# Kernel optimization log

Measured on AMD Instinct MI355X. Metric: run time of the kernel, lower is better.

The kernel has to match this reference:

```python
import jax, jax.numpy as jnp
import numpy as np

D = 128
K = 8
TEMPERATURE = 1.0
LN_EPS = 1e-5
NORM_EPS = 1e-12


def setup_inputs() -> dict:
    key = jax.random.key(0)
    ks = jax.random.split(key, 6)
    B = 262144
    global_prosody = jax.random.normal(ks[0], (B, D), dtype=jnp.float32)
    W = jax.random.normal(ks[1], (D, D), dtype=jnp.float32) / np.sqrt(D)
    b = jnp.zeros((D,), dtype=jnp.float32)
    gamma = jnp.ones((D,), dtype=jnp.float32)
    beta = jnp.zeros((D,), dtype=jnp.float32)
    # codebook initialized as rows of an orthonormal basis (SVD of random init)
    init = jax.random.normal(ks[2], (D, K), dtype=jnp.float32)
    U, _, _ = jnp.linalg.svd(init, full_matrices=False)
    codebook = U[:, :K].T  # (K, D)
    return {"global_prosody": global_prosody, "W": W, "b": b,
            "gamma": gamma, "beta": beta, "codebook": codebook}


def _l2norm(x, axis=-1):
    n = jnp.sqrt(jnp.sum(x * x, axis=axis, keepdims=True))
    return x / jnp.maximum(n, NORM_EPS)


def reference(global_prosody, W, b, gamma, beta, codebook):
    # proj: Linear + LayerNorm
    h = global_prosody @ W.T + b                      # (B, D)
    mu = jnp.mean(h, axis=-1, keepdims=True)
    var = jnp.var(h, axis=-1, keepdims=True)
    h = (h - mu) / jnp.sqrt(var + LN_EPS) * gamma + beta
    # cosine-sim logits
    h_norm = _l2norm(h)                               # (B, D)
    cb_norm = _l2norm(codebook)                       # (K, D)
    logits = (h_norm @ cb_norm.T) / TEMPERATURE       # (B, K)
    soft_assign = jax.nn.softmax(logits, axis=-1)
    hard_indices = jnp.argmax(logits, axis=-1)        # (B,)
    hard_assign = jax.nn.one_hot(hard_indices, K, dtype=jnp.float32)
    # straight-through assignment
    assign = hard_assign + soft_assign - jax.lax.stop_gradient(soft_assign)
    embedding = assign @ codebook                     # (B, D)
    return hard_indices, soft_assign, embedding, logits
```

## Files before the change

kernel.cpp:

```cpp
#include <hip/hip_runtime.h>
#include <math.h>

#define DD 128
#define KK 8
#define LN_EPS 1e-5f
#define NORM_EPS 1e-12f

typedef __attribute__((ext_vector_type(8))) short bf16x8;
typedef __attribute__((ext_vector_type(16))) float f32x16;
typedef unsigned int uint;
typedef unsigned short ushort;

#define G2B_OFF_F   (122880 / 4)
#define SCAL_OFF_F  (123904 / 4)

__device__ inline void split3(float x, uint& h, uint& m, uint& l) {
    uint u0 = __float_as_uint(x);
    uint rh = (u0 + 0x7FFFu + ((u0 >> 16) & 1u)) & 0xFFFF0000u;
    float xh = __uint_as_float(rh);
    float r1 = x - xh;
    uint u1 = __float_as_uint(r1);
    uint rm = (u1 + 0x7FFFu + ((u1 >> 16) & 1u)) & 0xFFFF0000u;
    float xm = __uint_as_float(rm);
    float r2 = r1 - xm;
    uint u2 = __float_as_uint(r2);
    uint rl = (u2 + 0x7FFFu + ((u2 >> 16) & 1u));
    h = rh; m = rm; l = rl;
}

__device__ inline void split3t(float x, uint& h, uint& m, uint& l) {
    uint u0 = __float_as_uint(x);
    float xh = __uint_as_float(u0 & 0xFFFF0000u);
    float r1 = x - xh;
    uint u1 = __float_as_uint(r1);
    float xm = __uint_as_float(u1 & 0xFFFF0000u);
    float r2 = r1 - xm;
    h = u0; m = u1; l = __float_as_uint(r2);
}

__device__ inline uint packhi(uint a1, uint a0) {
    return __builtin_amdgcn_perm(a1, a0, 0x07060302u);
}

__device__ inline void split2packt(float e0, float e1, uint& ph, uint& pm, uint& pl) {
    uint h0, m0, l0, h1, m1, l1;
    split3t(e0, h0, m0, l0);
    split3t(e1, h1, m1, l1);
    ph = packhi(h1, h0);
    pm = packhi(m1, m0);
    pl = packhi(l1, l0);
}

union FragU  { uint4 u; bf16x8 f; };
union AccU16 { f32x16 v; float a[16]; };

__global__ void l1q_prep0(const float* __restrict__ b, const float* __restrict__ gamma,
                          const float* __restrict__ beta, const float* __restrict__ cb,
                          float* __restrict__ ws)
{
    __shared__ float invn_s[KK];
    const int t = threadIdx.x;
    if (t < KK) {
        float s = 0.f;
        for (int j = 0; j < DD; ++j) { float v = cb[t * DD + j]; s = fmaf(v, v, s); }
        invn_s[t] = 1.0f / fmaxf(sqrtf(s), NORM_EPS);
    }
    __syncthreads();
    {
        float g = gamma[t];
        float* g2b = ws + G2B_OFF_F;
        g2b[2 * t]     = g * g;
        g2b[2 * t + 1] = b[t];
    }
    float* scal = ws + SCAL_OFF_F;
    if (t < KK) {
        float in = invn_s[t];
        float p = 0.f, q = 0.f, cu = 0.f;
        for (int j = 0; j < DD; ++j) {
            float c = cb[t * DD + j] * in;
            p  = fmaf(c, gamma[j], p);
            q  = fmaf(c, beta[j], q);
            cu = fmaf(c * gamma[j], b[j], cu);
        }
        scal[t]      = p;
        scal[8 + t]  = q;
        scal[22 + t] = cu;
    }
    if (t == 16) { float s = 0.f; for (int j = 0; j < DD; ++j) { float g = gamma[j]; s = fmaf(g, g, s); } scal[16] = s; }
    if (t == 17) { float s = 0.f; for (int j = 0; j < DD; ++j) s = fmaf(gamma[j], beta[j], s); scal[17] = s; }
    if (t == 18) { float s = 0.f; for (int j = 0; j < DD; ++j) { float v = beta[j]; s = fmaf(v, v, s); } scal[18] = s; }
    if (t == 19) { float s = 0.f; for (int j = 0; j < DD; ++j) s += b[j]; scal[19] = s; }
    if (t == 20) { float s = 0.f; for (int j = 0; j < DD; ++j) s = fmaf(gamma[j] * gamma[j], b[j], s); scal[20] = s; }
    if (t == 21) { float s = 0.f; for (int j = 0; j < DD; ++j) s = fmaf(gamma[j] * beta[j], b[j], s); scal[21] = s; }
}

__global__ void l1q_prepA(const float* __restrict__ W, const float* __restrict__ b,
                          const float* __restrict__ gamma, const float* __restrict__ beta,
                          const float* __restrict__ cb, ushort* __restrict__ wsA)
{
    __shared__ float invn_s[KK];
    __shared__ float we[11][DD];
    __shared__ float wext[32][16];
    const int t = threadIdx.x;
    const int jt = blockIdx.x >> 3;
    const int ks = blockIdx.x & 7;

    if (jt == 4) {
        if (t < KK) {
            float s = 0.f;
            for (int j = 0; j < DD; ++j) { float v = cb[t * DD + j]; s = fmaf(v, v, s); }
            invn_s[t] = 1.0f / fmaxf(sqrtf(s), NORM_EPS);
        }
        __syncthreads();
        for (int idx = t; idx < 11 * DD; idx += 256) {
            int e = idx / DD, j = idx % DD;
            float g = gamma[j];
            float v;
            if (e == 0)      v = 1.0f;
            else if (e == 1) v = g * g;
            else if (e == 2) v = g * beta[j];
            else             v = cb[(e - 3) * DD + j] * invn_s[e - 3] * g;
            we[e][j] = v;
        }
        __syncthreads();
    }

    for (int idx = t; idx < 512; idx += 256) {
        int jl = idx >> 4, kk = idx & 15;
        int k = ks * 16 + kk;
        float val;
        if (jt < 4) {
            val = W[(jt * 32 + jl) * DD + k];
        } else if (jl < 11) {
            float s = 0.f;
            for (int j = 0; j < DD; ++j) s = fmaf(we[jl][j], W[j * DD + k], s);
            val = s;
        } else {
            val = 0.f;
        }
        wext[jl][kk] = val;
    }
    __syncthreads();

    for (int idx = t; idx < 512; idx += 256) {
        int jl = idx >> 4, kk = idx & 15;
        int lane = jl + 32 * (kk >> 3);
        int i = kk & 7;
        uint h, m, l;
        split3(wext[jl][kk], h, m, l);
        int base = jt * 8 + ks;
        wsA[(0 * 40 + base) * 512 + lane * 8 + i] = (ushort)(h >> 16);
        wsA[(1 * 40 + base) * 512 + lane * 8 + i] = (ushort)(m >> 16);
        wsA[(2 * 40 + base) * 512 + lane * 8 + i] = (ushort)(l >> 16);
    }
}

__global__ __launch_bounds__(1024, 4)
void l1q_main(const float* __restrict__ x, const ushort* __restrict__ wsA,
              const float* __restrict__ wsf, const float* __restrict__ cb,
              float* __restrict__ out_idx, float* __restrict__ out_soft,
              float* __restrict__ out_emb, float* __restrict__ out_log,
              int B)
{
    __shared__ uint4 Wl4[7680];
    __shared__ float gath[16][352];
    __shared__ int   besti[16][32];
    __shared__ float g2b_s[256];
    __shared__ float scal_s[32];

    const int t = threadIdx.x;
    const int wave = t >> 6;
    const int lane = t & 63;
    const int n = lane & 31;
    const int h = lane >> 5;
    const int rowbase = blockIdx.x * 512 + wave * 32;
    const int row = rowbase + n;

    const float* xp = x + (size_t)row * DD + h * 8;
    float4 ra = *(const float4*)(xp + 0);
    float4 rc = *(const float4*)(xp + 4);

    {
        const uint4* src = (const uint4*)wsA;
        #pragma unroll
        for (int i = 0; i < 8; ++i) {
            int idx = t + i * 1024;
            if (idx < 7680) Wl4[idx] = src[idx];
        }
    }
    if (t < 256) g2b_s[t] = wsf[G2B_OFF_F + t];
    if (t < 32)  scal_s[t] = wsf[SCAL_OFF_F + t];
    __syncthreads();

    f32x16 acc[5];
    #pragma unroll
    for (int jt = 0; jt < 5; ++jt)
        #pragma unroll
        for (int r = 0; r < 16; ++r) acc[jt][r] = 0.f;

    #pragma unroll
    for (int ks = 0; ks < 8; ++ks) {
        int kn = ks < 7 ? ks + 1 : 7;
        float4 na = *(const float4*)(xp + kn * 16 + 0);
        float4 nc = *(const float4*)(xp + kn * 16 + 4);

        FragU xh, xm, xl;
        split2packt(ra.x, ra.y, xh.u.x, xm.u.x, xl.u.x);
        split2packt(ra.z, ra.w, xh.u.y, xm.u.y, xl.u.y);
        split2packt(rc.x, rc.y, xh.u.z, xm.u.z, xl.u.z);
        split2packt(rc.z, rc.w, xh.u.w, xm.u.w, xl.u.w);

        #pragma unroll
        for (int jt = 0; jt < 5; ++jt) {
            const int pl = jt * 8 + ks;
            FragU wh, wm, wl;
            wh.u = Wl4[(0 * 40 + pl) * 64 + lane];
            wm.u = Wl4[(1 * 40 + pl) * 64 + lane];
            wl.u = Wl4[(2 * 40 + pl) * 64 + lane];
            f32x16 c = acc[jt];
            c = __builtin_amdgcn_mfma_f32_32x32x16_bf16(wl.f, xh.f, c, 0, 0, 0);
            c = __builtin_amdgcn_mfma_f32_32x32x16_bf16(wh.f, xl.f, c, 0, 0, 0);
            c = __builtin_amdgcn_mfma_f32_32x32x16_bf16(wm.f, xm.f, c, 0, 0, 0);
            c = __builtin_amdgcn_mfma_f32_32x32x16_bf16(wm.f, xh.f, c, 0, 0, 0);
            c = __builtin_amdgcn_mfma_f32_32x32x16_bf16(wh.f, xm.f, c, 0, 0, 0);
            c = __builtin_amdgcn_mfma_f32_32x32x16_bf16(wh.f, xh.f, c, 0, 0, 0);
            acc[jt] = c;
        }
        ra = na; rc = nc;
    }

    float s2a = 0.f, t2a = 0.f;
    #pragma unroll
    for (int jt = 0; jt < 4; ++jt) {
        AccU16 a; a.v = acc[jt];
        #pragma unroll
        for (int rq = 0; rq < 4; ++rq) {
            int jb = jt * 32 + 8 * rq + 4 * h;
            #pragma unroll
            for (int r = 0; r < 4; ++r) {
                float2 gb = *(const float2*)&g2b_s[2 * (jb + r)];
                float hv = a.a[rq * 4 + r] + gb.y;
                float h2 = hv * hv;
                s2a += h2;
                t2a = fmaf(gb.x, h2, t2a);
            }
        }
    }
    s2a += __shfl_xor(s2a, 32);
    t2a += __shfl_xor(t2a, 32);

    {
        AccU16 a; a.v = acc[4];
        #pragma unroll
        for (int rq = 0; rq < 4; ++rq) {
            #pragma unroll
            for (int r = 0; r < 4; ++r) {
                int local = r + 8 * rq + 4 * h;
                if (local < 11) gath[wave][n * 11 + local] = a.a[rq * 4 + r];
            }
        }
    }
    __builtin_amdgcn_s_waitcnt(0);
    const float* gp = &gath[wave][n * 11];

    const float inv128 = 1.0f / 128.0f;
    const float cg2s = scal_s[16], cgbs = scal_s[17], cb2s = scal_s[18];

    float s1  = gp[0] + scal_s[19];
    float t1  = gp[1] + scal_s[20];
    float r1v = gp[2] + scal_s[21];
    float u[KK];
    #pragma unroll
    for (int k = 0; k < KK; ++k) u[k] = gp[3 + k] + scal_s[22 + k];

    float mu = s1 * inv128;
    float var = fmaf(-mu, mu, s2a * inv128);
    float istd = 1.0f / sqrtf(var + LN_EPS);
    float nrm2 = istd * istd * (t2a - 2.f * mu * t1 + mu * mu * cg2s)
               + 2.f * istd * (r1v - mu * cgbs) + cb2s;
    float rinv = 1.0f / fmaxf(sqrtf(fmaxf(nrm2, 0.f)), NORM_EPS);

    float lg[KK];
    #pragma unroll
    for (int k = 0; k < KK; ++k)
        lg[k] = (istd * (u[k] - mu * scal_s[k]) + scal_s[8 + k]) * rinv;

    float mx = lg[0]; int bi = 0;
    #pragma unroll
    for (int k = 1; k < KK; ++k) if (lg[k] > mx) { mx = lg[k]; bi = k; }

    float ex[KK], se = 0.f;
    #pragma unroll
    for (int k = 0; k < KK; ++k) { ex[k] = expf(lg[k] - mx); se += ex[k]; }
    float rse = 1.0f / se;

    const int m = rowbase + n;
    if (h == 0) {
        out_idx[m] = (float)bi;
        besti[wave][n] = bi;
        *(float4*)&out_log[(size_t)m * KK]     = make_float4(lg[0], lg[1], lg[2], lg[3]);
        *(float4*)&out_log[(size_t)m * KK + 4] = make_float4(lg[4], lg[5], lg[6], lg[7]);
    } else {
        *(float4*)&out_soft[(size_t)m * KK]     = make_float4(ex[0] * rse, ex[1] * rse, ex[2] * rse, ex[3] * rse);
        *(float4*)&out_soft[(size_t)m * KK + 4] = make_float4(ex[4] * rse, ex[5] * rse, ex[6] * rse, ex[7] * rse);
    }

    __builtin_amdgcn_s_waitcnt(0);
    const float4* cb4 = (const float4*)cb;
    float4* eo = (float4*)out_emb;
    #pragma unroll
    for (int i = 0; i < 16; ++i) {
        int f4 = lane + 64 * i;
        int rl = f4 >> 5;
        int c  = f4 & 31;
        int k0 = besti[wave][rl];
        eo[(size_t)(rowbase + rl) * 32 + c] = cb4[k0 * 32 + c];
    }
}

extern "C" void kernel_launch(void* const* d_in, const int* in_sizes, int n_in,
                              void* d_out, int out_size, void* d_ws, size_t ws_size,
                              hipStream_t stream) {
    const float* x     = (const float*)d_in[0];
    const float* W     = (const float*)d_in[1];
    const float* b     = (const float*)d_in[2];
    const float* gamma = (const float*)d_in[3];
    const float* beta  = (const float*)d_in[4];
    const float* cb    = (const float*)d_in[5];
    const int B = in_sizes[0] / DD;

    float*  ws  = (float*)d_ws;
    ushort* wsA = (ushort*)d_ws;

    float* out    = (float*)d_out;
    float* o_idx  = out;
    float* o_soft = out + (size_t)B;
    float* o_emb  = out + (size_t)B * (1 + KK);
    float* o_log  = out + (size_t)B * (1 + KK + DD);

    hipLaunchKernelGGL(l1q_prep0, dim3(1), dim3(128), 0, stream, b, gamma, beta, cb, ws);
    hipLaunchKernelGGL(l1q_prepA, dim3(40), dim3(256), 0, stream, W, b, gamma, beta, cb, wsA);
    const int grid = B / 512;
    hipLaunchKernelGGL(l1q_main, dim3(grid), dim3(1024), 0, stream,
                       x, wsA, ws, cb, o_idx, o_soft, o_emb, o_log, B);
}
```

Baseline: 297.7 us.

## Process two row tiles per wave, sharing W fragments, and fold prep kernels

Each wave now handles 64 rows as two 32-row tiles, so every W fragment read from LDS feeds two interleaved MFMA chains. All x loads are issued up front, and the grid is halved, which spreads the LDS W staging over twice as many rows. The epilogue swaps the LDS gather and the besti scratch for cross-lane shuffles, and the scalar-prep kernel is merged into prepA to save a launch. The cost is much higher register pressure from 32 float4 x registers plus two accumulator sets, which risks spills or lower occupancy. Fewer blocks also means less latency hiding across blocks.

```diff
diff --git a/kernel.cpp b/kernel.cpp
--- a/kernel.cpp
+++ b/kernel.cpp
@@ -52,51 +52,11 @@
 }
 
 union FragU  { uint4 u; bf16x8 f; };
-union AccU16 { f32x16 v; float a[16]; };
-
-__global__ void l1q_prep0(const float* __restrict__ b, const float* __restrict__ gamma,
-                          const float* __restrict__ beta, const float* __restrict__ cb,
-                          float* __restrict__ ws)
-{
-    __shared__ float invn_s[KK];
-    const int t = threadIdx.x;
-    if (t < KK) {
-        float s = 0.f;
-        for (int j = 0; j < DD; ++j) { float v = cb[t * DD + j]; s = fmaf(v, v, s); }
-        invn_s[t] = 1.0f / fmaxf(sqrtf(s), NORM_EPS);
-    }
-    __syncthreads();
-    {
-        float g = gamma[t];
-        float* g2b = ws + G2B_OFF_F;
-        g2b[2 * t]     = g * g;
-        g2b[2 * t + 1] = b[t];
-    }
-    float* scal = ws + SCAL_OFF_F;
-    if (t < KK) {
-        float in = invn_s[t];
-        float p = 0.f, q = 0.f, cu = 0.f;
-        for (int j = 0; j < DD; ++j) {
-            float c = cb[t * DD + j] * in;
-            p  = fmaf(c, gamma[j], p);
-            q  = fmaf(c, beta[j], q);
-            cu = fmaf(c * gamma[j], b[j], cu);
-        }
-        scal[t]      = p;
-        scal[8 + t]  = q;
-        scal[22 + t] = cu;
-    }
-    if (t == 16) { float s = 0.f; for (int j = 0; j < DD; ++j) { float g = gamma[j]; s = fmaf(g, g, s); } scal[16] = s; }
-    if (t == 17) { float s = 0.f; for (int j = 0; j < DD; ++j) s = fmaf(gamma[j], beta[j], s); scal[17] = s; }
-    if (t == 18) { float s = 0.f; for (int j = 0; j < DD; ++j) { float v = beta[j]; s = fmaf(v, v, s); } scal[18] = s; }
-    if (t == 19) { float s = 0.f; for (int j = 0; j < DD; ++j) s += b[j]; scal[19] = s; }
-    if (t == 20) { float s = 0.f; for (int j = 0; j < DD; ++j) s = fmaf(gamma[j] * gamma[j], b[j], s); scal[20] = s; }
-    if (t == 21) { float s = 0.f; for (int j = 0; j < DD; ++j) s = fmaf(gamma[j] * beta[j], b[j], s); scal[21] = s; }
-}
 
 __global__ void l1q_prepA(const float* __restrict__ W, const float* __restrict__ b,
                           const float* __restrict__ gamma, const float* __restrict__ beta,
-                          const float* __restrict__ cb, ushort* __restrict__ wsA)
+                          const float* __restrict__ cb, ushort* __restrict__ wsA,
+                          float* __restrict__ ws)
 {
     __shared__ float invn_s[KK];
     __shared__ float we[11][DD];
@@ -153,6 +113,112 @@
         wsA[(1 * 40 + base) * 512 + lane * 8 + i] = (ushort)(m >> 16);
         wsA[(2 * 40 + base) * 512 + lane * 8 + i] = (ushort)(l >> 16);
     }
+
+    if (jt == 4 && ks == 0) {
+        if (t < DD) {
+            float g = gamma[t];
+            float* g2b = ws + G2B_OFF_F;
+            g2b[2 * t]     = g * g;
+            g2b[2 * t + 1] = b[t];
+        }
+        float* scal = ws + SCAL_OFF_F;
+        if (t < KK) {
+            float in = invn_s[t];
+            float p = 0.f, q = 0.f, cu = 0.f;
+            for (int j = 0; j < DD; ++j) {
+                float c = cb[t * DD + j] * in;
+                p  = fmaf(c, gamma[j], p);
+                q  = fmaf(c, beta[j], q);
+                cu = fmaf(c * gamma[j], b[j], cu);
+            }
+            scal[t]      = p;
+            scal[8 + t]  = q;
+            scal[22 + t] = cu;
+        }
+        if (t == 16) { float s = 0.f; for (int j = 0; j < DD; ++j) { float g = gamma[j]; s = fmaf(g, g, s); } scal[16] = s; }
+        if (t == 17) { float s = 0.f; for (int j = 0; j < DD; ++j) s = fmaf(gamma[j], beta[j], s); scal[17] = s; }
+        if (t == 18) { float s = 0.f; for (int j = 0; j < DD; ++j) { float v = beta[j]; s = fmaf(v, v, s); } scal[18] = s; }
+        if (t == 19) { float s = 0.f; for (int j = 0; j < DD; ++j) s += b[j]; scal[19] = s; }
+        if (t == 20) { float s = 0.f; for (int j = 0; j < DD; ++j) s = fmaf(gamma[j] * gamma[j], b[j], s); scal[20] = s; }
+        if (t == 21) { float s = 0.f; for (int j = 0; j < DD; ++j) s = fmaf(gamma[j] * beta[j], b[j], s); scal[21] = s; }
+    }
+}
+
+__device__ inline int tile_epilogue(const f32x16* acc, int h, int m,
+                                    const float* g2b_s, const float* scal_s,
+                                    float* __restrict__ out_idx,
+                                    float* __restrict__ out_soft,
+                                    float* __restrict__ out_log)
+{
+    float s2a = 0.f, t2a = 0.f;
+    #pragma unroll
+    for (int jt = 0; jt < 4; ++jt) {
+        #pragma unroll
+        for (int rq = 0; rq < 4; ++rq) {
+            int jb = jt * 32 + 8 * rq + 4 * h;
+            #pragma unroll
+            for (int r = 0; r < 4; ++r) {
+                float2 gb = *(const float2*)&g2b_s[2 * (jb + r)];
+                float hv = acc[jt][rq * 4 + r] + gb.y;
+                float h2 = hv * hv;
+                s2a += h2;
+                t2a = fmaf(gb.x, h2, t2a);
+            }
+        }
+    }
+    s2a += __shfl_xor(s2a, 32);
+    t2a += __shfl_xor(t2a, 32);
+
+    float a0 = acc[4][0], a1 = acc[4][1], a2 = acc[4][2], a3 = acc[4][3];
+    float a4 = acc[4][4], a5 = acc[4][5], a6 = acc[4][6];
+    float o0 = __shfl_xor(a0, 32), o1 = __shfl_xor(a1, 32);
+    float o2 = __shfl_xor(a2, 32), o3 = __shfl_xor(a3, 32);
+    float o4 = __shfl_xor(a4, 32), o5 = __shfl_xor(a5, 32), o6 = __shfl_xor(a6, 32);
+    bool hi = (h != 0);
+    float L0 = hi ? o0 : a0, L1 = hi ? o1 : a1, L2 = hi ? o2 : a2, L3 = hi ? o3 : a3;
+    float L4 = hi ? a0 : o0, L5 = hi ? a1 : o1, L6 = hi ? a2 : o2, L7 = hi ? a3 : o3;
+    float L8 = hi ? o4 : a4, L9 = hi ? o5 : a5, L10 = hi ? o6 : a6;
+
+    const float inv128 = 1.0f / 128.0f;
+    const float cg2s = scal_s[16], cgbs = scal_s[17], cb2s = scal_s[18];
+
+    float s1  = L0 + scal_s[19];
+    float t1  = L1 + scal_s[20];
+    float r1v = L2 + scal_s[21];
+    float u[KK] = {L3 + scal_s[22], L4 + scal_s[23], L5 + scal_s[24],
+                   L6 + scal_s[25], L7 + scal_s[26], L8 + scal_s[27],
+                   L9 + scal_s[28], L10 + scal_s[29]};
+
+    float mu = s1 * inv128;
+    float var = fmaf(-mu, mu, s2a * inv128);
+    float istd = 1.0f / sqrtf(var + LN_EPS);
+    float nrm2 = istd * istd * (t2a - 2.f * mu * t1 + mu * mu * cg2s)
+               + 2.f * istd * (r1v - mu * cgbs) + cb2s;
+    float rinv = 1.0f / fmaxf(sqrtf(fmaxf(nrm2, 0.f)), NORM_EPS);
+
+    float lg[KK];
+    #pragma unroll
+    for (int k = 0; k < KK; ++k)
+        lg[k] = (istd * (u[k] - mu * scal_s[k]) + scal_s[8 + k]) * rinv;
+
+    float mx = lg[0]; int bi = 0;
+    #pragma unroll
+    for (int k = 1; k < KK; ++k) if (lg[k] > mx) { mx = lg[k]; bi = k; }
+
+    float ex[KK], se = 0.f;
+    #pragma unroll
+    for (int k = 0; k < KK; ++k) { ex[k] = expf(lg[k] - mx); se += ex[k]; }
+    float rse = 1.0f / se;
+
+    if (h == 0) {
+        out_idx[m] = (float)bi;
+        *(float4*)&out_log[(size_t)m * KK]     = make_float4(lg[0], lg[1], lg[2], lg[3]);
+        *(float4*)&out_log[(size_t)m * KK + 4] = make_float4(lg[4], lg[5], lg[6], lg[7]);
+    } else {
+        *(float4*)&out_soft[(size_t)m * KK]     = make_float4(ex[0] * rse, ex[1] * rse, ex[2] * rse, ex[3] * rse);
+        *(float4*)&out_soft[(size_t)m * KK + 4] = make_float4(ex[4] * rse, ex[5] * rse, ex[6] * rse, ex[7] * rse);
+    }
+    return bi;
 }
 
 __global__ __launch_bounds__(1024, 4)
@@ -163,22 +229,15 @@
               int B)
 {
     __shared__ uint4 Wl4[7680];
-    __shared__ float gath[16][352];
-    __shared__ int   besti[16][32];
     __shared__ float g2b_s[256];
     __shared__ float scal_s[32];
 
     const int t = threadIdx.x;
+    const int lane = t & 63;
     const int wave = t >> 6;
-    const int lane = t & 63;
     const int n = lane & 31;
     const int h = lane >> 5;
-    const int rowbase = blockIdx.x * 512 + wave * 32;
-    const int row = rowbase + n;
-
-    const float* xp = x + (size_t)row * DD + h * 8;
-    float4 ra = *(const float4*)(xp + 0);
-    float4 rc = *(const float4*)(xp + 4);
+    const int rowbase = blockIdx.x * 1024 + wave * 64;
 
     {
         const uint4* src = (const uint4*)wsA;
@@ -192,23 +251,34 @@
     if (t < 32)  scal_s[t] = wsf[SCAL_OFF_F + t];
     __syncthreads();
 
-    f32x16 acc[5];
+    const float* xpA = x + (size_t)(rowbase + n) * DD + h * 8;
+    const float* xpB = xpA + 32 * DD;
+    float4 xA[16], xB[16];
+    #pragma unroll
+    for (int ks = 0; ks < 8; ++ks) {
+        xA[2 * ks]     = *(const float4*)(xpA + ks * 16);
+        xA[2 * ks + 1] = *(const float4*)(xpA + ks * 16 + 4);
+        xB[2 * ks]     = *(const float4*)(xpB + ks * 16);
+        xB[2 * ks + 1] = *(const float4*)(xpB + ks * 16 + 4);
+    }
+
+    f32x16 accA[5], accB[5];
     #pragma unroll
     for (int jt = 0; jt < 5; ++jt)
         #pragma unroll
-        for (int r = 0; r < 16; ++r) acc[jt][r] = 0.f;
+        for (int r = 0; r < 16; ++r) { accA[jt][r] = 0.f; accB[jt][r] = 0.f; }
 
     #pragma unroll
     for (int ks = 0; ks < 8; ++ks) {
-        int kn = ks < 7 ? ks + 1 : 7;
-        float4 na = *(const float4*)(xp + kn * 16 + 0);
-        float4 nc = *(const float4*)(xp + kn * 16 + 4);
-
-        FragU xh, xm, xl;
-        split2packt(ra.x, ra.y, xh.u.x, xm.u.x, xl.u.x);
-        split2packt(ra.z, ra.w, xh.u.y, xm.u.y, xl.u.y);
-        split2packt(rc.x, rc.y, xh.u.z, xm.u.z, xl.u.z);
-        split2packt(rc.z, rc.w, xh.u.w, xm.u.w, xl.u.w);
+        FragU ah, am, al, bh, bm, bl;
+        split2packt(xA[2 * ks].x,     xA[2 * ks].y,     ah.u.x, am.u.x, al.u.x);
+        split2packt(xA[2 * ks].z,     xA[2 * ks].w,     ah.u.y, am.u.y, al.u.y);
+        split2packt(xA[2 * ks + 1].x, xA[2 * ks + 1].y, ah.u.z, am.u.z, al.u.z);
+        split2packt(xA[2 * ks + 1].z, xA[2 * ks + 1].w, ah.u.w, am.u.w, al.u.w);
+        split2packt(xB[2 * ks].x,     xB[2 * ks].y,     bh.u.x, bm.u.x, bl.u.x);
+        split2packt(xB[2 * ks].z,     xB[2 * ks].w,     bh.u.y, bm.u.y, bl.u.y);
+        split2packt(xB[2 * ks + 1].x, xB[2 * ks + 1].y, bh.u.z, bm.u.z, bl.u.z);
+        split2packt(xB[2 * ks + 1].z, xB[2 * ks + 1].w, bh.u.w, bm.u.w, bl.u.w);
 
         #pragma unroll
         for (int jt = 0; jt < 5; ++jt) {
@@ -217,95 +287,27 @@
             wh.u = Wl4[(0 * 40 + pl) * 64 + lane];
             wm.u = Wl4[(1 * 40 + pl) * 64 + lane];
             wl.u = Wl4[(2 * 40 + pl) * 64 + lane];
-            f32x16 c = acc[jt];
-            c = __builtin_amdgcn_mfma_f32_32x32x16_bf16(wl.f, xh.f, c, 0, 0, 0);
-            c = __builtin_amdgcn_mfma_f32_32x32x16_bf16(wh.f, xl.f, c, 0, 0, 0);
-            c = __builtin_amdgcn_mfma_f32_32x32x16_bf16(wm.f, xm.f, c, 0, 0, 0);
-            c = __builtin_amdgcn_mfma_f32_32x32x16_bf16(wm.f, xh.f, c, 0, 0, 0);
-            c = __builtin_amdgcn_mfma_f32_32x32x16_bf16(wh.f, xm.f, c, 0, 0, 0);
-            c = __builtin_amdgcn_mfma_f32_32x32x16_bf16(wh.f, xh.f, c, 0, 0, 0);
-            acc[jt] = c;
-        }
-        ra = na; rc = nc;
-    }
-
-    float s2a = 0.f, t2a = 0.f;
-    #pragma unroll
-    for (int jt = 0; jt < 4; ++jt) {
-        AccU16 a; a.v = acc[jt];
-        #pragma unroll
-        for (int rq = 0; rq < 4; ++rq) {
-            int jb = jt * 32 + 8 * rq + 4 * h;
-            #pragma unroll
-            for (int r = 0; r < 4; ++r) {
-                float2 gb = *(const float2*)&g2b_s[2 * (jb + r)];
-                float hv = a.a[rq * 4 + r] + gb.y;
-                float h2 = hv * hv;
-                s2a += h2;
-                t2a = fmaf(gb.x, h2, t2a);
-            }
-        }
-    }
-    s2a += __shfl_xor(s2a, 32);
-    t2a += __shfl_xor(t2a, 32);
-
-    {
-        AccU16 a; a.v = acc[4];
-        #pragma unroll
-        for (int rq = 0; rq < 4; ++rq) {
-            #pragma unroll
-            for (int r = 0; r < 4; ++r) {
-                int local = r + 8 * rq + 4 * h;
-                if (local < 11) gath[wave][n * 11 + local] = a.a[rq * 4 + r];
-            }
-        }
-    }
-    __builtin_amdgcn_s_waitcnt(0);
-    const float* gp = &gath[wave][n * 11];
-
-    const float inv128 = 1.0f / 128.0f;
-    const float cg2s = scal_s[16], cgbs = scal_s[17], cb2s = scal_s[18];
-
-    float s1  = gp[0] + scal_s[19];
-    float t1  = gp[1] + scal_s[20];
-    float r1v = gp[2] + scal_s[21];
-    float u[KK];
-    #pragma unroll
-    for (int k = 0; k < KK; ++k) u[k] = gp[3 + k] + scal_s[22 + k];
-
-    float mu = s1 * inv128;
-    float var = fmaf(-mu, mu, s2a * inv128);
-    float istd = 1.0f / sqrtf(var + LN_EPS);
-    float nrm2 = istd * istd * (t2a - 2.f * mu * t1 + mu * mu * cg2s)
-               + 2.f * istd * (r1v - mu * cgbs) + cb2s;
-    float rinv = 1.0f / fmaxf(sqrtf(fmaxf(nrm2, 0.f)), NORM_EPS);
-
-    float lg[KK];
-    #pragma unroll
-    for (int k = 0; k < KK; ++k)
-        lg[k] = (istd * (u[k] - mu * scal_s[k]) + scal_s[8 + k]) * rinv;
-
-    float mx = lg[0]; int bi = 0;
-    #pragma unroll
-    for (int k = 1; k < KK; ++k) if (lg[k] > mx) { mx = lg[k]; bi = k; }
-
-    float ex[KK], se = 0.f;
-    #pragma unroll
-    for (int k = 0; k < KK; ++k) { ex[k] = expf(lg[k] - mx); se += ex[k]; }
-    float rse = 1.0f / se;
-
-    const int m = rowbase + n;
-    if (h == 0) {
-        out_idx[m] = (float)bi;
-        besti[wave][n] = bi;
-        *(float4*)&out_log[(size_t)m * KK]     = make_float4(lg[0], lg[1], lg[2], lg[3]);
-        *(float4*)&out_log[(size_t)m * KK + 4] = make_float4(lg[4], lg[5], lg[6], lg[7]);
-    } else {
-        *(float4*)&out_soft[(size_t)m * KK]     = make_float4(ex[0] * rse, ex[1] * rse, ex[2] * rse, ex[3] * rse);
-        *(float4*)&out_soft[(size_t)m * KK + 4] = make_float4(ex[4] * rse, ex[5] * rse, ex[6] * rse, ex[7] * rse);
-    }
-
-    __builtin_amdgcn_s_waitcnt(0);
+            f32x16 cA = accA[jt], cB = accB[jt];
+            cA = __builtin_amdgcn_mfma_f32_32x32x16_bf16(wl.f, ah.f, cA, 0, 0, 0);
+            cB = __builtin_amdgcn_mfma_f32_32x32x16_bf16(wl.f, bh.f, cB, 0, 0, 0);
+            cA = __builtin_amdgcn_mfma_f32_32x32x16_bf16(wh.f, al.f, cA, 0, 0, 0);
+            cB = __builtin_amdgcn_mfma_f32_32x32x16_bf16(wh.f, bl.f, cB, 0, 0, 0);
+            cA = __builtin_amdgcn_mfma_f32_32x32x16_bf16(wm.f, am.f, cA, 0, 0, 0);
+            cB = __builtin_amdgcn_mfma_f32_32x32x16_bf16(wm.f, bm.f, cB, 0, 0, 0);
+            cA = __builtin_amdgcn_mfma_f32_32x32x16_bf16(wm.f, ah.f, cA, 0, 0, 0);
+            cB = __builtin_amdgcn_mfma_f32_32x32x16_bf16(wm.f, bh.f, cB, 0, 0, 0);
+            cA = __builtin_amdgcn_mfma_f32_32x32x16_bf16(wh.f, am.f, cA, 0, 0, 0);
+            cB = __builtin_amdgcn_mfma_f32_32x32x16_bf16(wh.f, bm.f, cB, 0, 0, 0);
+            cA = __builtin_amdgcn_mfma_f32_32x32x16_bf16(wh.f, ah.f, cA, 0, 0, 0);
+            cB = __builtin_amdgcn_mfma_f32_32x32x16_bf16(wh.f, bh.f, cB, 0, 0, 0);
+            accA[jt] = cA; accB[jt] = cB;
+        }
+    }
+
+    const int mA = rowbase + n;
+    int bA = tile_epilogue(accA, h, mA, g2b_s, scal_s, out_idx, out_soft, out_log);
+    int bB = tile_epilogue(accB, h, mA + 32, g2b_s, scal_s, out_idx, out_soft, out_log);
+
     const float4* cb4 = (const float4*)cb;
     float4* eo = (float4*)out_emb;
     #pragma unroll
@@ -313,8 +315,16 @@
         int f4 = lane + 64 * i;
         int rl = f4 >> 5;
         int c  = f4 & 31;
-        int k0 = besti[wave][rl];
-        eo[(size_t)(rowbase + rl) * 32 + c] = cb4[k0 * 32 + c];
+        int kA = __shfl(bA, rl);
+        eo[(size_t)(rowbase + rl) * 32 + c] = cb4[kA * 32 + c];
+    }
+    #pragma unroll
+    for (int i = 0; i < 16; ++i) {
+        int f4 = lane + 64 * i;
+        int rl = f4 >> 5;
+        int c  = f4 & 31;
+        int kB = __shfl(bB, rl);
+        eo[(size_t)(rowbase + 32 + rl) * 32 + c] = cb4[kB * 32 + c];
     }
 }
 
@@ -338,9 +348,8 @@
     float* o_emb  = out + (size_t)B * (1 + KK);
     float* o_log  = out + (size_t)B * (1 + KK + DD);
 
-    hipLaunchKernelGGL(l1q_prep0, dim3(1), dim3(128), 0, stream, b, gamma, beta, cb, ws);
-    hipLaunchKernelGGL(l1q_prepA, dim3(40), dim3(256), 0, stream, W, b, gamma, beta, cb, wsA);
-    const int grid = B / 512;
+    hipLaunchKernelGGL(l1q_prepA, dim3(40), dim3(256), 0, stream, W, b, gamma, beta, cb, wsA, ws);
+    const int grid = B / 1024;
     hipLaunchKernelGGL(l1q_main, dim3(grid), dim3(1024), 0, stream,
                        x, wsA, ws, cb, o_idx, o_soft, o_emb, o_log, B);
 }
```

After: 837.2 us. +181.3%, slower.
